# Performance work log

Hardware: AMD Instinct MI355X
Metric: run time of the kernel (lower is better)

The kernel has to match this reference:

```python
import jax, jax.numpy as jnp
import numpy as np

D_MODEL = 512; D_STATE = 256; D_CONV = 2; EXPAND = 1; D_FF = 1024
D_INNER = EXPAND * D_MODEL
DT_RANK = (D_MODEL + 15) // 16  # ceil(d_model/16), mamba_ssm convention
B = 8; L = 2048


def setup_inputs() -> dict:
    key = jax.random.key(0)
    ks = jax.random.split(key, 10)
    g = lambda i, shape, sc: jax.random.normal(ks[i], shape, jnp.float32) * sc
    return {
        'x_tokens': g(0, (B, L, D_MODEL), 1.0),
        'in_proj_w': g(1, (2 * D_INNER, D_MODEL), D_MODEL ** -0.5),
        'conv_w': g(2, (D_INNER, 1, D_CONV), D_CONV ** -0.5),
        'conv_b': jnp.zeros((D_INNER,), jnp.float32),
        'x_proj_w': g(3, (DT_RANK + 2 * D_STATE, D_INNER), D_INNER ** -0.5),
        'dt_proj_w': g(4, (D_INNER, DT_RANK), DT_RANK ** -0.5),
        'dt_proj_b': jnp.full((D_INNER,), -4.6, jnp.float32),  # softplus(-4.6)~0.01
        'A_log': jnp.log(jnp.broadcast_to(jnp.arange(1, D_STATE + 1, dtype=jnp.float32), (D_INNER, D_STATE))),
        'D_skip': jnp.ones((D_INNER,), jnp.float32),
        'out_proj_w': g(5, (D_MODEL, D_INNER), D_INNER ** -0.5),
        'ln1_g': jnp.ones((D_MODEL,), jnp.float32),
        'ln1_b': jnp.zeros((D_MODEL,), jnp.float32),
        'ffn_w1': g(6, (D_FF, D_MODEL), D_MODEL ** -0.5),
        'ffn_b1': jnp.zeros((D_FF,), jnp.float32),
        'ffn_w2': g(7, (D_MODEL, D_FF), D_FF ** -0.5),
        'ffn_b2': jnp.zeros((D_MODEL,), jnp.float32),
        'ln2_g': jnp.ones((D_MODEL,), jnp.float32),
        'ln2_b': jnp.zeros((D_MODEL,), jnp.float32),
    }


def _layer_norm(x, g, b, eps=1e-5):
    mu = jnp.mean(x, axis=-1, keepdims=True)
    var = jnp.mean(jnp.square(x - mu), axis=-1, keepdims=True)
    return (x - mu) * jax.lax.rsqrt(var + eps) * g + b


def _mamba(x, in_proj_w, conv_w, conv_b, x_proj_w, dt_proj_w, dt_proj_b, A_log, D_skip, out_proj_w):
    bsz = x.shape[0]
    xz = x @ in_proj_w.T                                  # (B, L, 2*d_inner)
    xs, z = jnp.split(xz, 2, axis=-1)
    # depthwise causal conv1d, width d_conv
    xc = jnp.transpose(xs, (0, 2, 1))                     # (B, d_inner, L)
    xc = jax.lax.conv_general_dilated(
        xc, conv_w, window_strides=(1,), padding=[(D_CONV - 1, 0)],
        dimension_numbers=('NCH', 'OIH', 'NCH'), feature_group_count=D_INNER)
    xs = jax.nn.silu(jnp.transpose(xc, (0, 2, 1)) + conv_b)  # (B, L, d_inner)
    # input-dependent dt, B, C
    dbl = xs @ x_proj_w.T
    dtl, Bm, Cm = jnp.split(dbl, [DT_RANK, DT_RANK + D_STATE], axis=-1)
    dt = jax.nn.softplus(dtl @ dt_proj_w.T + dt_proj_b)   # (B, L, d_inner)
    A = -jnp.exp(A_log)                                   # (d_inner, d_state)

    def step(h, inp):
        dt_t, B_t, C_t, x_t = inp                         # (B,d_in),(B,N),(B,N),(B,d_in)
        h = jnp.exp(dt_t[:, :, None] * A) * h + (dt_t * x_t)[:, :, None] * B_t[:, None, :]
        y_t = jnp.einsum('bdn,bn->bd', h, C_t)
        return h, y_t

    h0 = jnp.zeros((bsz, D_INNER, D_STATE), x.dtype)
    seq = (jnp.transpose(dt, (1, 0, 2)), jnp.transpose(Bm, (1, 0, 2)),
           jnp.transpose(Cm, (1, 0, 2)), jnp.transpose(xs, (1, 0, 2)))
    _, ys = jax.lax.scan(step, h0, seq)                   # ys: (L, B, d_inner)
    y = jnp.transpose(ys, (1, 0, 2)) + xs * D_skip
    y = y * jax.nn.silu(z)
    return y @ out_proj_w.T


def reference(x_tokens, in_proj_w, conv_w, conv_b, x_proj_w, dt_proj_w, dt_proj_b,
              A_log, D_skip, out_proj_w, ln1_g, ln1_b, ffn_w1, ffn_b1, ffn_w2, ffn_b2,
              ln2_g, ln2_b):
    y = _mamba(x_tokens, in_proj_w, conv_w, conv_b, x_proj_w, dt_proj_w, dt_proj_b,
               A_log, D_skip, out_proj_w)
    x = _layer_norm(x_tokens + y, ln1_g, ln1_b)
    y = jax.nn.relu(x @ ffn_w1.T + ffn_b1) @ ffn_w2.T + ffn_b2  # dropout off (eval)
    return _layer_norm(x + y, ln2_g, ln2_b)
```

## Files before the change

### kernel.cpp

```cpp
#include <hip/hip_runtime.h>
#include <hip/hip_bf16.h>
#include <math.h>

#define SEQ     2048
#define NROWS   16384
#define DBL_N   544

typedef __attribute__((ext_vector_type(8))) short bf16x8;
typedef __attribute__((ext_vector_type(4))) float f32x4;
typedef __attribute__((ext_vector_type(2))) float f32x2;

static __device__ __forceinline__ unsigned short f2bf(float x) {
    __hip_bfloat16 h = __float2bfloat16(x);
    return *reinterpret_cast<unsigned short*>(&h);
}

static __device__ __forceinline__ float rdlane(float v, int l) {
    return __int_as_float(__builtin_amdgcn_readlane(__float_as_int(v), l));
}

template<int EPI>
__global__ __launch_bounds__(256, 2)
void gemm_bf16(const float* __restrict__ A, int lda,
               const float* __restrict__ W, int ldw,
               const float* __restrict__ bias,
               float* __restrict__ out, int ldo,
               int N, int K)
{
    __shared__ short Asl[4 * 128 * 8];
    __shared__ short Wsl[4 * 128 * 8];
    const int t  = threadIdx.x;
    const int m0 = blockIdx.y * 128, n0 = blockIdx.x * 128;
    const int wv = t >> 6;
    const int wm = (wv & 1) * 64;
    const int wn = (wv >> 1) * 64;
    const int ln = t & 63;
    const int lq = ln >> 4;
    const int lc = ln & 15;
    const int lr  = t >> 1;
    const int lk4 = (t & 1) * 4;
    const int arow = m0 + lr;
    const int wrow = n0 + lr;
    const bool wok = wrow < N;

    f32x4 acc[4][4];
    #pragma unroll
    for (int i = 0; i < 4; ++i)
        #pragma unroll
        for (int j = 0; j < 4; ++j)
            acc[i][j] = (f32x4){0.f, 0.f, 0.f, 0.f};

    for (int k0 = 0; k0 < K; k0 += 32) {
        float4 av[4], wv4[4];
        #pragma unroll
        for (int ks = 0; ks < 4; ++ks) {
            av[ks] = *reinterpret_cast<const float4*>(A + (size_t)arow * lda + k0 + ks * 8 + lk4);
            wv4[ks] = wok ? *reinterpret_cast<const float4*>(W + (size_t)wrow * ldw + k0 + ks * 8 + lk4)
                          : make_float4(0.f, 0.f, 0.f, 0.f);
        }
        __syncthreads();
        #pragma unroll
        for (int ks = 0; ks < 4; ++ks) {
            ushort4 ap, wp;
            ap.x = f2bf(av[ks].x);  ap.y = f2bf(av[ks].y);
            ap.z = f2bf(av[ks].z);  ap.w = f2bf(av[ks].w);
            wp.x = f2bf(wv4[ks].x); wp.y = f2bf(wv4[ks].y);
            wp.z = f2bf(wv4[ks].z); wp.w = f2bf(wv4[ks].w);
            *reinterpret_cast<ushort4*>(&Asl[(ks * 128 + lr) * 8 + lk4]) = ap;
            *reinterpret_cast<ushort4*>(&Wsl[(ks * 128 + lr) * 8 + lk4]) = wp;
        }
        __syncthreads();
        bf16x8 af[4], wf[4];
        #pragma unroll
        for (int i = 0; i < 4; ++i)
            af[i] = *reinterpret_cast<const bf16x8*>(&Asl[(lq * 128 + wm + i * 16 + lc) * 8]);
        #pragma unroll
        for (int j = 0; j < 4; ++j)
            wf[j] = *reinterpret_cast<const bf16x8*>(&Wsl[(lq * 128 + wn + j * 16 + lc) * 8]);
        #pragma unroll
        for (int i = 0; i < 4; ++i)
            #pragma unroll
            for (int j = 0; j < 4; ++j)
                acc[i][j] = __builtin_amdgcn_mfma_f32_16x16x32_bf16(af[i], wf[j], acc[i][j], 0, 0, 0);
    }

    float bvv[4];
    #pragma unroll
    for (int j = 0; j < 4; ++j) {
        int n = n0 + wn + j * 16 + lc;
        bvv[j] = (EPI >= 1 && n < N) ? bias[n] : 0.f;
    }
    #pragma unroll
    for (int i = 0; i < 4; ++i) {
        #pragma unroll
        for (int r = 0; r < 4; ++r) {
            const int m = m0 + wm + i * 16 + lq * 4 + r;
            #pragma unroll
            for (int j = 0; j < 4; ++j) {
                const int n = n0 + wn + j * 16 + lc;
                float x = acc[i][j][r];
                if (EPI >= 1) x += bvv[j];
                if (EPI == 1) x = fmaxf(x, 0.f);
                if (n < N) out[(size_t)m * ldo + n] = x;
            }
        }
    }
}

template<int EPI>
__global__ __launch_bounds__(256, 2)
void gemm_nt(const float* __restrict__ A, int lda,
             const float* __restrict__ W, int ldw,
             const float* __restrict__ bias,
             float* __restrict__ out, int ldo,
             int N, int K)
{
    __shared__ float As[8][132];
    __shared__ float Ws[8][132];
    const int t  = threadIdx.x;
    const int tx = t & 15, ty = t >> 4;
    const int m0 = blockIdx.y * 128, n0 = blockIdx.x * 128;
    const int lr = t >> 1, lc = (t & 1) * 4;
    const int arow = m0 + lr;
    const int wrow = n0 + lr;
    const bool wok = wrow < N;

    float acc[8][8];
    #pragma unroll
    for (int i = 0; i < 8; ++i)
        #pragma unroll
        for (int j = 0; j < 8; ++j) acc[i][j] = 0.f;

    for (int k0 = 0; k0 < K; k0 += 8) {
        float av[4], wv[4] = {0.f, 0.f, 0.f, 0.f};
        {
            float4 v = *reinterpret_cast<const float4*>(A + (size_t)arow * lda + k0 + lc);
            av[0] = v.x; av[1] = v.y; av[2] = v.z; av[3] = v.w;
        }
        if (wok) {
            float4 v = *reinterpret_cast<const float4*>(W + (size_t)wrow * ldw + k0 + lc);
            wv[0] = v.x; wv[1] = v.y; wv[2] = v.z; wv[3] = v.w;
        }
        __syncthreads();
        #pragma unroll
        for (int i = 0; i < 4; ++i) { As[lc + i][lr] = av[i]; Ws[lc + i][lr] = wv[i]; }
        __syncthreads();
        #pragma unroll
        for (int kk = 0; kk < 8; ++kk) {
            float a[8], bb[8];
            *reinterpret_cast<float4*>(a)      = *reinterpret_cast<const float4*>(&As[kk][ty * 8]);
            *reinterpret_cast<float4*>(a + 4)  = *reinterpret_cast<const float4*>(&As[kk][ty * 8 + 4]);
            *reinterpret_cast<float4*>(bb)     = *reinterpret_cast<const float4*>(&Ws[kk][tx * 8]);
            *reinterpret_cast<float4*>(bb + 4) = *reinterpret_cast<const float4*>(&Ws[kk][tx * 8 + 4]);
            #pragma unroll
            for (int i = 0; i < 8; ++i)
                #pragma unroll
                for (int j = 0; j < 8; ++j)
                    acc[i][j] = fmaf(a[i], bb[j], acc[i][j]);
        }
    }

    float bv[8];
    #pragma unroll
    for (int j = 0; j < 8; ++j) {
        int n = n0 + tx * 8 + j;
        bv[j] = (EPI >= 1 && n < N) ? bias[n] : 0.f;
    }
    #pragma unroll
    for (int i = 0; i < 8; ++i) {
        int m = m0 + ty * 8 + i;
        float v[8];
        #pragma unroll
        for (int j = 0; j < 8; ++j) {
            float x = acc[i][j];
            if (EPI >= 1) x += bv[j];
            if (EPI == 1) x = fmaxf(x, 0.f);
            if (EPI == 2) x = (x > 20.f) ? x : log1pf(expf(x));
            v[j] = x;
        }
        float* op = out + (size_t)m * ldo + n0 + tx * 8;
        if (n0 + 128 <= N) {
            *reinterpret_cast<float4*>(op)     = make_float4(v[0], v[1], v[2], v[3]);
            *reinterpret_cast<float4*>(op + 4) = make_float4(v[4], v[5], v[6], v[7]);
        } else {
            #pragma unroll
            for (int j = 0; j < 8; ++j)
                if (n0 + tx * 8 + j < N) op[j] = v[j];
        }
    }
}

__global__ __launch_bounds__(256)
void conv_silu(const float* __restrict__ xz, const float* __restrict__ cw,
               const float* __restrict__ cb, float* __restrict__ xs)
{
    int idx = blockIdx.x * 256 + threadIdx.x;
    int c   = idx & 511;
    int row = idx >> 9;
    int l   = row & (SEQ - 1);
    float v = cw[2 * c + 1] * xz[(size_t)row * 1024 + c] + cb[c];
    if (l > 0) v += cw[2 * c] * xz[(size_t)(row - 1) * 1024 + c];
    xs[idx] = v / (1.f + __expf(-v));
}

__global__ __launch_bounds__(256)
void init_a2(const float* __restrict__ A_log, float* __restrict__ A2)
{
    int i = blockIdx.x * 256 + threadIdx.x;
    A2[i] = -__expf(A_log[i]);
}

#define TB 16
__global__ __launch_bounds__(512, 4)
void ssm_scan(const float* __restrict__ dbl, const float* __restrict__ dtp,
              const float* __restrict__ xs, const float* __restrict__ zp,
              const float* __restrict__ A2, const float* __restrict__ Dskip,
              float* __restrict__ ygate)
{
    const int t  = threadIdx.x;
    const int b  = blockIdx.x & 7;
    const int d0 = (blockIdx.x >> 3) * 8;
    const int w  = t >> 6;
    const int ln = t & 63;
    const int n0 = ln * 4;
    const int c  = d0 + w;
    const size_t rbase = (size_t)b * SEQ;

    __shared__ float Bs[2][TB][256];
    __shared__ float Cs[2][TB][256];

    f32x2 h0 = {0.f, 0.f}, h1 = {0.f, 0.f};

    const float aA  = A2[c * 256 + n0] * 1.44269504f;
    const float dl2 = (A2[c * 256 + 1] - A2[c * 256]) * 1.44269504f;
    const float Dv  = Dskip[c];

    const int  half = ln >> 5;
    const int  c4   = (ln & 31) * 4;
    const int  scol = 32 + half * 256;
    const int  sg   = ln >> 2;
    const bool gok  = (ln & 3) == 0;

    float dtg = 0.f, xg = 0.f, zg = 0.f;
    {
        #pragma unroll
        for (int r2 = 0; r2 < 2; ++r2) {
            const int row = w + r2 * 8;
            const size_t g = (rbase + row) * 544;
            float4 v0 = *reinterpret_cast<const float4*>(dbl + g + scol + c4);
            float4 v1 = *reinterpret_cast<const float4*>(dbl + g + scol + c4 + 128);
            float* dst = half ? &Cs[0][row][0] : &Bs[0][row][0];
            *reinterpret_cast<float4*>(dst + c4)       = v0;
            *reinterpret_cast<float4*>(dst + c4 + 128) = v1;
        }
        if (gok) {
            dtg = dtp[(rbase + sg) * 1024 + c];
            xg  = xs [(rbase + sg) * 512  + c];
            zg  = zp [(rbase + sg) * 1024 + c];
        }
    }
    __syncthreads();

    for (int sup = 0; sup < SEQ / TB; ++sup) {
        const int cur = sup & 1;
        const int ts  = sup * TB;
        const bool more = (sup + 1 < SEQ / TB);

        float4 p00, p01, p10, p11;
        float pdt = 0.f, pxv = 0.f, pzv = 0.f;
        if (more) {
            const size_t g0 = (rbase + ts + TB + w) * 544;
            const size_t g1 = (rbase + ts + TB + w + 8) * 544;
            p00 = *reinterpret_cast<const float4*>(dbl + g0 + scol + c4);
            p01 = *reinterpret_cast<const float4*>(dbl + g0 + scol + c4 + 128);
            p10 = *reinterpret_cast<const float4*>(dbl + g1 + scol + c4);
            p11 = *reinterpret_cast<const float4*>(dbl + g1 + scol + c4 + 128);
            if (gok) {
                pdt = dtp[(rbase + ts + TB + sg) * 1024 + c];
                pxv = xs [(rbase + ts + TB + sg) * 512  + c];
                pzv = zp [(rbase + ts + TB + sg) * 1024 + c];
            }
        }

        const float rvg  = __builtin_amdgcn_exp2f(dtg * dl2);
        const float dtxg = dtg * xg;

        float part[TB];
        #pragma unroll
        for (int s = 0; s < TB; ++s) {
            const float sdt  = rdlane(dtg,  4 * s);
            const float sdtx = rdlane(dtxg, 4 * s);
            const float srv  = rdlane(rvg,  4 * s);
            const f32x4 Bq = *reinterpret_cast<const f32x4*>(&Bs[cur][s][n0]);
            const f32x4 Cq = *reinterpret_cast<const f32x4*>(&Cs[cur][s][n0]);
            const f32x2 B01 = {Bq.x, Bq.y}, B23 = {Bq.z, Bq.w};
            const f32x2 C01 = {Cq.x, Cq.y}, C23 = {Cq.z, Cq.w};
            const float e0  = __builtin_amdgcn_exp2f(sdt * aA);
            const float e1  = e0 * srv;
            const float srv2 = srv * srv;
            const f32x2 e01 = {e0, e1};
            const f32x2 e23 = e01 * srv2;
            h0 = __builtin_elementwise_fma(e01, h0, B01 * sdtx);
            h1 = __builtin_elementwise_fma(e23, h1, B23 * sdtx);
            f32x2 p = h0 * C01;
            p = __builtin_elementwise_fma(h1, C23, p);
            part[s] = p.x + p.y;
        }

        float v;
        {
            const bool lo5 = (ln & 32) == 0;
            const bool lo4 = (ln & 16) == 0;
            const bool lo3 = (ln & 8) == 0;
            const bool lo2 = (ln & 4) == 0;
            float q[8];
            #pragma unroll
            for (int k = 0; k < 8; ++k) {
                float send = lo5 ? part[k + 8] : part[k];
                float keep = lo5 ? part[k]     : part[k + 8];
                q[k] = keep + __shfl_xor(send, 32, 64);
            }
            float u[4];
            #pragma unroll
            for (int k = 0; k < 4; ++k) {
                float send = lo4 ? q[k + 4] : q[k];
                float keep = lo4 ? q[k]     : q[k + 4];
                u[k] = keep + __shfl_xor(send, 16, 64);
            }
            float w2[2];
            #pragma unroll
            for (int k = 0; k < 2; ++k) {
                float send = lo3 ? u[k + 2] : u[k];
                float keep = lo3 ? u[k]     : u[k + 2];
                w2[k] = keep + __shfl_xor(send, 8, 64);
            }
            float send = lo2 ? w2[1] : w2[0];
            float keep = lo2 ? w2[0] : w2[1];
            v = keep + __shfl_xor(send, 4, 64);
            v += __shfl_xor(v, 2, 64);
            v += __shfl_xor(v, 1, 64);
        }

        {
            const float yt   = fmaf(xg, Dv, v);
            const float gate = zg / (1.f + __expf(-zg));
            if (gok) ygate[(rbase + ts + sg) * 512 + c] = yt * gate;
        }

        if (more) {
            const int nxt = cur ^ 1;
            float* dst0 = half ? &Cs[nxt][w][0]     : &Bs[nxt][w][0];
            float* dst1 = half ? &Cs[nxt][w + 8][0] : &Bs[nxt][w + 8][0];
            *reinterpret_cast<float4*>(dst0 + c4)       = p00;
            *reinterpret_cast<float4*>(dst0 + c4 + 128) = p01;
            *reinterpret_cast<float4*>(dst1 + c4)       = p10;
            *reinterpret_cast<float4*>(dst1 + c4 + 128) = p11;
            dtg = pdt; xg = pxv; zg = pzv;
        }
        __syncthreads();
    }
}

__global__ __launch_bounds__(64)
void add_ln(const float* __restrict__ in1, const float* __restrict__ in2,
            const float* __restrict__ g, const float* __restrict__ bb,
            float* __restrict__ out)
{
    const int row = blockIdx.x;
    const int t   = threadIdx.x;
    float v[8];
    #pragma unroll
    for (int k = 0; k < 8; ++k) {
        int c = t + 64 * k;
        size_t ix = (size_t)row * 512 + c;
        v[k] = in1[ix] + in2[ix];
    }
    float s = 0.f;
    #pragma unroll
    for (int k = 0; k < 8; ++k) s += v[k];
    #pragma unroll
    for (int off = 32; off >= 1; off >>= 1) s += __shfl_xor(s, off, 64);
    float mean = s * (1.f / 512.f);
    float q = 0.f;
    #pragma unroll
    for (int k = 0; k < 8; ++k) { float dd = v[k] - mean; q += dd * dd; }
    #pragma unroll
    for (int off = 32; off >= 1; off >>= 1) q += __shfl_xor(q, off, 64);
    float rstd = rsqrtf(q * (1.f / 512.f) + 1e-5f);
    #pragma unroll
    for (int k = 0; k < 8; ++k) {
        int c = t + 64 * k;
        size_t ix = (size_t)row * 512 + c;
        out[ix] = (v[k] - mean) * rstd * g[c] + bb[c];
    }
}

extern "C" void kernel_launch(void* const* d_in, const int* in_sizes, int n_in,
                              void* d_out, int out_size, void* d_ws, size_t ws_size,
                              hipStream_t stream)
{
    (void)in_sizes; (void)n_in; (void)out_size; (void)ws_size;
    const float* x_tokens   = (const float*)d_in[0];
    const float* in_proj_w  = (const float*)d_in[1];
    const float* conv_w     = (const float*)d_in[2];
    const float* conv_b     = (const float*)d_in[3];
    const float* x_proj_w   = (const float*)d_in[4];
    const float* dt_proj_w  = (const float*)d_in[5];
    const float* dt_proj_b  = (const float*)d_in[6];
    const float* A_log      = (const float*)d_in[7];
    const float* D_skip     = (const float*)d_in[8];
    const float* out_proj_w = (const float*)d_in[9];
    const float* ln1_g      = (const float*)d_in[10];
    const float* ln1_b      = (const float*)d_in[11];
    const float* ffn_w1     = (const float*)d_in[12];
    const float* ffn_b1     = (const float*)d_in[13];
    const float* ffn_w2     = (const float*)d_in[14];
    const float* ffn_b2     = (const float*)d_in[15];
    const float* ln2_g      = (const float*)d_in[16];
    const float* ln2_b      = (const float*)d_in[17];

    float* ws    = (float*)d_ws;
    float* A2    = ws;
    float* xz    = A2   + 131072;
    float* dbl   = xz   + 16777216;
    float* xs    = dbl  + 8912896;
    float* ygate = xs   + 8388608;
    float* dtb   = xz;
    float* yo    = dbl;
    float* x1    = xs;
    float* hffn  = xz;
    float* yo2   = ygate;

    hipLaunchKernelGGL(init_a2, dim3(512), dim3(256), 0, stream, A_log, A2);
    hipLaunchKernelGGL((gemm_bf16<0>), dim3(8, 128), dim3(256), 0, stream,
                       x_tokens, 512, in_proj_w, 512, (const float*)nullptr,
                       xz, 1024, 1024, 512);
    hipLaunchKernelGGL(conv_silu, dim3(NROWS * 512 / 256), dim3(256), 0, stream,
                       xz, conv_w, conv_b, xs);
    hipLaunchKernelGGL((gemm_bf16<0>), dim3(5, 128), dim3(256), 0, stream,
                       xs, 512, x_proj_w, 512, (const float*)nullptr,
                       dbl, DBL_N, DBL_N, 512);
    hipLaunchKernelGGL((gemm_nt<2>), dim3(4, 128), dim3(256), 0, stream,
                       dbl, DBL_N, dt_proj_w, 32, dt_proj_b,
                       dtb, 1024, 512, 32);
    hipLaunchKernelGGL(ssm_scan, dim3(512), dim3(512), 0, stream,
                       dbl, dtb, xs, xz + 512, A2, D_skip, ygate);
    hipLaunchKernelGGL((gemm_bf16<0>), dim3(4, 128), dim3(256), 0, stream,
                       ygate, 512, out_proj_w, 512, (const float*)nullptr,
                       yo, 512, 512, 512);
    hipLaunchKernelGGL(add_ln, dim3(NROWS), dim3(64), 0, stream,
                       x_tokens, yo, ln1_g, ln1_b, x1);
    hipLaunchKernelGGL((gemm_bf16<1>), dim3(8, 128), dim3(256), 0, stream,
                       x1, 512, ffn_w1, 512, ffn_b1, hffn, 1024, 1024, 512);
    hipLaunchKernelGGL((gemm_bf16<3>), dim3(4, 128), dim3(256), 0, stream,
                       hffn, 1024, ffn_w2, 1024, ffn_b2, yo2, 512, 512, 1024);
    hipLaunchKernelGGL(add_ln, dim3(NROWS), dim3(64), 0, stream,
                       x1, yo2, ln2_g, ln2_b, (float*)d_out);
}
```

Before: 921.7 us.

## Pre-convert GEMM operands to bf16 and stage tiles via global_load_lds

```diff
diff --git a/kernel.cpp b/kernel.cpp
--- a/kernel.cpp
+++ b/kernel.cpp
@@ -9,6 +9,7 @@
 typedef __attribute__((ext_vector_type(8))) short bf16x8;
 typedef __attribute__((ext_vector_type(4))) float f32x4;
 typedef __attribute__((ext_vector_type(2))) float f32x2;
+typedef unsigned short ushort_t;
 
 static __device__ __forceinline__ unsigned short f2bf(float x) {
     __hip_bfloat16 h = __float2bfloat16(x);
@@ -19,13 +20,31 @@
     return __int_as_float(__builtin_amdgcn_readlane(__float_as_int(v), l));
 }
 
-template<int EPI>
+static __device__ __forceinline__ void gload16(const unsigned short* g, short* l) {
+    typedef const __attribute__((address_space(1))) unsigned int* gp_t;
+    typedef __attribute__((address_space(3))) unsigned int* sp_t;
+    __builtin_amdgcn_global_load_lds((gp_t)(const void*)g, (sp_t)(void*)l, 16, 0, 0);
+}
+
+__global__ __launch_bounds__(256)
+void cvt_bf(const float* __restrict__ src, unsigned short* __restrict__ dst, int n)
+{
+    int i = (blockIdx.x * 256 + threadIdx.x) * 4;
+    if (i < n) {
+        float4 v = *reinterpret_cast<const float4*>(src + i);
+        ushort4 o;
+        o.x = f2bf(v.x); o.y = f2bf(v.y); o.z = f2bf(v.z); o.w = f2bf(v.w);
+        *reinterpret_cast<ushort4*>(dst + i) = o;
+    }
+}
+
+template<int EPI, int OBF>
 __global__ __launch_bounds__(256, 2)
-void gemm_bf16(const float* __restrict__ A, int lda,
-               const float* __restrict__ W, int ldw,
-               const float* __restrict__ bias,
-               float* __restrict__ out, int ldo,
-               int N, int K)
+void gemm_bb(const unsigned short* __restrict__ A, int lda,
+             const unsigned short* __restrict__ W, int ldw,
+             const float* __restrict__ bias,
+             float* __restrict__ out, int ldo,
+             int N, int K)
 {
     __shared__ short Asl[4 * 128 * 8];
     __shared__ short Wsl[4 * 128 * 8];
@@ -37,11 +56,21 @@
     const int ln = t & 63;
     const int lq = ln >> 4;
     const int lc = ln & 15;
-    const int lr  = t >> 1;
-    const int lk4 = (t & 1) * 4;
-    const int arow = m0 + lr;
-    const int wrow = n0 + lr;
-    const bool wok = wrow < N;
+
+    const int q0  = t >> 7;
+    const int row = t & 127;
+    const int arow = m0 + row;
+    const int wr   = n0 + row;
+    const int wrow = (wr < N) ? wr : (N - 1);
+    const unsigned short* ga0 = A + (size_t)arow * lda + q0 * 8;
+    const unsigned short* ga1 = ga0 + 16;
+    const unsigned short* gw0 = W + (size_t)wrow * ldw + q0 * 8;
+    const unsigned short* gw1 = gw0 + 16;
+    const int wb = (t & ~63);
+    short* asl0 = &Asl[wb * 8];
+    short* asl1 = &Asl[(wb + 256) * 8];
+    short* wsl0 = &Wsl[wb * 8];
+    short* wsl1 = &Wsl[(wb + 256) * 8];
 
     f32x4 acc[4][4];
     #pragma unroll
@@ -51,25 +80,13 @@
             acc[i][j] = (f32x4){0.f, 0.f, 0.f, 0.f};
 
     for (int k0 = 0; k0 < K; k0 += 32) {
-        float4 av[4], wv4[4];
-        #pragma unroll
-        for (int ks = 0; ks < 4; ++ks) {
-            av[ks] = *reinterpret_cast<const float4*>(A + (size_t)arow * lda + k0 + ks * 8 + lk4);
-            wv4[ks] = wok ? *reinterpret_cast<const float4*>(W + (size_t)wrow * ldw + k0 + ks * 8 + lk4)
-                          : make_float4(0.f, 0.f, 0.f, 0.f);
-        }
         __syncthreads();
-        #pragma unroll
-        for (int ks = 0; ks < 4; ++ks) {
-            ushort4 ap, wp;
-            ap.x = f2bf(av[ks].x);  ap.y = f2bf(av[ks].y);
-            ap.z = f2bf(av[ks].z);  ap.w = f2bf(av[ks].w);
-            wp.x = f2bf(wv4[ks].x); wp.y = f2bf(wv4[ks].y);
-            wp.z = f2bf(wv4[ks].z); wp.w = f2bf(wv4[ks].w);
-            *reinterpret_cast<ushort4*>(&Asl[(ks * 128 + lr) * 8 + lk4]) = ap;
-            *reinterpret_cast<ushort4*>(&Wsl[(ks * 128 + lr) * 8 + lk4]) = wp;
-        }
+        gload16(ga0 + k0, asl0);
+        gload16(ga1 + k0, asl1);
+        gload16(gw0 + k0, wsl0);
+        gload16(gw1 + k0, wsl1);
         __syncthreads();
+
         bf16x8 af[4], wf[4];
         #pragma unroll
         for (int i = 0; i < 4; ++i)
@@ -90,6 +107,7 @@
         int n = n0 + wn + j * 16 + lc;
         bvv[j] = (EPI >= 1 && n < N) ? bias[n] : 0.f;
     }
+    unsigned short* outb = reinterpret_cast<unsigned short*>(out);
     #pragma unroll
     for (int i = 0; i < 4; ++i) {
         #pragma unroll
@@ -101,7 +119,10 @@
                 float x = acc[i][j][r];
                 if (EPI >= 1) x += bvv[j];
                 if (EPI == 1) x = fmaxf(x, 0.f);
-                if (n < N) out[(size_t)m * ldo + n] = x;
+                if (n < N) {
+                    if (OBF) outb[(size_t)m * ldo + n] = f2bf(x);
+                    else     out[(size_t)m * ldo + n]  = x;
+                }
             }
         }
     }
@@ -192,7 +213,8 @@
 
 __global__ __launch_bounds__(256)
 void conv_silu(const float* __restrict__ xz, const float* __restrict__ cw,
-               const float* __restrict__ cb, float* __restrict__ xs)
+               const float* __restrict__ cb, float* __restrict__ xs,
+               unsigned short* __restrict__ xs_bf)
 {
     int idx = blockIdx.x * 256 + threadIdx.x;
     int c   = idx & 511;
@@ -200,7 +222,9 @@
     int l   = row & (SEQ - 1);
     float v = cw[2 * c + 1] * xz[(size_t)row * 1024 + c] + cb[c];
     if (l > 0) v += cw[2 * c] * xz[(size_t)(row - 1) * 1024 + c];
-    xs[idx] = v / (1.f + __expf(-v));
+    float sv = v / (1.f + __expf(-v));
+    xs[idx]    = sv;
+    xs_bf[idx] = f2bf(sv);
 }
 
 __global__ __launch_bounds__(256)
@@ -215,7 +239,7 @@
 void ssm_scan(const float* __restrict__ dbl, const float* __restrict__ dtp,
               const float* __restrict__ xs, const float* __restrict__ zp,
               const float* __restrict__ A2, const float* __restrict__ Dskip,
-              float* __restrict__ ygate)
+              unsigned short* __restrict__ ygate)
 {
     const int t  = threadIdx.x;
     const int b  = blockIdx.x & 7;
@@ -344,7 +368,7 @@
         {
             const float yt   = fmaf(xg, Dv, v);
             const float gate = zg / (1.f + __expf(-zg));
-            if (gok) ygate[(rbase + ts + sg) * 512 + c] = yt * gate;
+            if (gok) ygate[(rbase + ts + sg) * 512 + c] = f2bf(yt * gate);
         }
 
         if (more) {
@@ -361,10 +385,11 @@
     }
 }
 
+template<int OBF>
 __global__ __launch_bounds__(64)
 void add_ln(const float* __restrict__ in1, const float* __restrict__ in2,
             const float* __restrict__ g, const float* __restrict__ bb,
-            float* __restrict__ out)
+            float* __restrict__ out, unsigned short* __restrict__ obf)
 {
     const int row = blockIdx.x;
     const int t   = threadIdx.x;
@@ -391,7 +416,9 @@
     for (int k = 0; k < 8; ++k) {
         int c = t + 64 * k;
         size_t ix = (size_t)row * 512 + c;
-        out[ix] = (v[k] - mean) * rstd * g[c] + bb[c];
+        float o = (v[k] - mean) * rstd * g[c] + bb[c];
+        out[ix] = o;
+        if (OBF) obf[ix] = f2bf(o);
     }
 }
 
@@ -421,39 +448,51 @@
 
     float* ws    = (float*)d_ws;
     float* A2    = ws;
-    float* xz    = A2   + 131072;
-    float* dbl   = xz   + 16777216;
-    float* xs    = dbl  + 8912896;
-    float* ygate = xs   + 8388608;
+    float* xz    = A2  + 131072;
+    float* dbl   = xz  + 16777216;
+    float* xs    = dbl + 8912896;
+    unsigned short* ub   = (unsigned short*)(ws + 34209792);
+    unsigned short* abf  = ub;
+    unsigned short* w_in = ub + 8388608;
+    unsigned short* w_xp = w_in + 524288;
+    unsigned short* w_op = w_xp + 278528;
+    unsigned short* w_f1 = w_op + 262144;
+    unsigned short* w_f2 = w_f1 + 524288;
     float* dtb   = xz;
     float* yo    = dbl;
     float* x1    = xs;
-    float* hffn  = xz;
-    float* yo2   = ygate;
+    unsigned short* hffn = (unsigned short*)xz;
+    float* yo2   = dbl;
 
     hipLaunchKernelGGL(init_a2, dim3(512), dim3(256), 0, stream, A_log, A2);
-    hipLaunchKernelGGL((gemm_bf16<0>), dim3(8, 128), dim3(256), 0, stream,
-                       x_tokens, 512, in_proj_w, 512, (const float*)nullptr,
+    hipLaunchKernelGGL(cvt_bf, dim3(8192), dim3(256), 0, stream, x_tokens,  abf,  8388608);
+    hipLaunchKernelGGL(cvt_bf, dim3(512),  dim3(256), 0, stream, in_proj_w, w_in, 524288);
+    hipLaunchKernelGGL(cvt_bf, dim3(272),  dim3(256), 0, stream, x_proj_w,  w_xp, 278528);
+    hipLaunchKernelGGL(cvt_bf, dim3(256),  dim3(256), 0, stream, out_proj_w,w_op, 262144);
+    hipLaunchKernelGGL(cvt_bf, dim3(512),  dim3(256), 0, stream, ffn_w1,    w_f1, 524288);
+    hipLaunchKernelGGL(cvt_bf, dim3(512),  dim3(256), 0, stream, ffn_w2,    w_f2, 524288);
+    hipLaunchKernelGGL((gemm_bb<0,0>), dim3(8, 128), dim3(256), 0, stream,
+                       abf, 512, w_in, 512, (const float*)nullptr,
                        xz, 1024, 1024, 512);
     hipLaunchKernelGGL(conv_silu, dim3(NROWS * 512 / 256), dim3(256), 0, stream,
-                       xz, conv_w, conv_b, xs);
-    hipLaunchKernelGGL((gemm_bf16<0>), dim3(5, 128), dim3(256), 0, stream,
-                       xs, 512, x_proj_w, 512, (const float*)nullptr,
+                       xz, conv_w, conv_b, xs, abf);
+    hipLaunchKernelGGL((gemm_bb<0,0>), dim3(5, 128), dim3(256), 0, stream,
+                       abf, 512, w_xp, 512, (const float*)nullptr,
                        dbl, DBL_N, DBL_N, 512);
     hipLaunchKernelGGL((gemm_nt<2>), dim3(4, 128), dim3(256), 0, stream,
                        dbl, DBL_N, dt_proj_w, 32, dt_proj_b,
                        dtb, 1024, 512, 32);
     hipLaunchKernelGGL(ssm_scan, dim3(512), dim3(512), 0, stream,
-                       dbl, dtb, xs, xz + 512, A2, D_skip, ygate);
-    hipLaunchKernelGGL((gemm_bf16<0>), dim3(4, 128), dim3(256), 0, stream,
-                       ygate, 512, out_proj_w, 512, (const float*)nullptr,
+                       dbl, dtb, xs, xz + 512, A2, D_skip, abf);
+    hipLaunchKernelGGL((gemm_bb<0,0>), dim3(4, 128), dim3(256), 0, stream,
+                       abf, 512, w_op, 512, (const float*)nullptr,
                        yo, 512, 512, 512);
-    hipLaunchKernelGGL(add_ln, dim3(NROWS), dim3(64), 0, stream,
-                       x_tokens, yo, ln1_g, ln1_b, x1);
-    hipLaunchKernelGGL((gemm_bf16<1>), dim3(8, 128), dim3(256), 0, stream,
-                       x1, 512, ffn_w1, 512, ffn_b1, hffn, 1024, 1024, 512);
-    hipLaunchKernelGGL((gemm_bf16<3>), dim3(4, 128), dim3(256), 0, stream,
-                       hffn, 1024, ffn_w2, 1024, ffn_b2, yo2, 512, 512, 1024);
-    hipLaunchKernelGGL(add_ln, dim3(NROWS), dim3(64), 0, stream,
-                       x1, yo2, ln2_g, ln2_b, (float*)d_out);
-}
+    hipLaunchKernelGGL((add_ln<1>), dim3(NROWS), dim3(64), 0, stream,
+                       x_tokens, yo, ln1_g, ln1_b, x1, abf);
+    hipLaunchKernelGGL((gemm_bb<1,1>), dim3(8, 128), dim3(256), 0, stream,
+                       abf, 512, w_f1, 512, ffn_b1, (float*)hffn, 1024, 1024, 512);
+    hipLaunchKernelGGL((gemm_bb<3,0>), dim3(4, 128), dim3(256), 0, stream,
+                       hffn, 1024, w_f2, 1024, ffn_b2, yo2, 512, 512, 1024);
+    hipLaunchKernelGGL((add_ln<0>), dim3(NROWS), dim3(64), 0, stream,
+                       x1, yo2, ln2_g, ln2_b, (float*)d_out, (unsigned short*)nullptr);
+}
```

Result: faster. 834.9 us (-9.4%).
